# Kernel tuning notes

Measured on AMD Instinct MI355X. Metric: run time of the kernel, lower is better.

Reference implementation:

```python
import jax, jax.numpy as jnp
import numpy as np

B, BARS, BEATS, FRAC = 64, 16, 4, 8
IN_F = 10 * 47 * 2  # 940
LIN_OUT = 100
BEAT_H = 16
BAR_H = 32


def _p(key, shape, scale=0.05):
    return jax.random.normal(key, shape, dtype=jnp.float32) * scale


def setup_inputs() -> dict:
    key = jax.random.key(0)
    ks = jax.random.split(key, 16)
    return {
        "channels": jax.random.normal(ks[0], (B, BARS, BEATS, FRAC, 10, 2, 47), dtype=jnp.float32),
        "lin_w": _p(ks[1], (LIN_OUT, IN_F)),
        "lin_b": _p(ks[2], (LIN_OUT,)),
        # beats LSTM (unidirectional), PyTorch gate order i,f,g,o
        "b_wih": _p(ks[3], (4 * BEAT_H, LIN_OUT)),
        "b_whh": _p(ks[4], (4 * BEAT_H, BEAT_H)),
        "b_bih": _p(ks[5], (4 * BEAT_H,)),
        "b_bhh": _p(ks[6], (4 * BEAT_H,)),
        # bars LSTM, bidirectional: forward (f_) and reverse (r_) directions
        "f_wih": _p(ks[7], (4 * BAR_H, BEAT_H)),
        "f_whh": _p(ks[8], (4 * BAR_H, BAR_H)),
        "f_bih": _p(ks[9], (4 * BAR_H,)),
        "f_bhh": _p(ks[10], (4 * BAR_H,)),
        "r_wih": _p(ks[11], (4 * BAR_H, BEAT_H)),
        "r_whh": _p(ks[12], (4 * BAR_H, BAR_H)),
        "r_bih": _p(ks[13], (4 * BAR_H,)),
        "r_bhh": _p(ks[14], (4 * BAR_H,)),
    }


def lstm(x, wih, whh, bih, bhh):
    """PyTorch-semantics LSTM, batch_first. x: [N, T, F] -> h_seq [N, T, H]."""
    N = x.shape[0]
    H = whh.shape[1]
    # precompute input contribution for all timesteps
    xg = jnp.einsum('ntf,gf->ntg', x, wih) + (bih + bhh)  # [N, T, 4H]

    def step(carry, xt):
        h, c = carry
        gates = xt + h @ whh.T  # [N, 4H]
        i, f, g, o = jnp.split(gates, 4, axis=-1)
        c = jax.nn.sigmoid(f) * c + jax.nn.sigmoid(i) * jnp.tanh(g)
        h = jax.nn.sigmoid(o) * jnp.tanh(c)
        return (h, c), h

    h0 = jnp.zeros((N, H), x.dtype)
    _, hs = jax.lax.scan(step, (h0, h0), jnp.swapaxes(xg, 0, 1))  # [T, N, H]
    return jnp.swapaxes(hs, 0, 1)


def bilstm(x, f_wih, f_whh, f_bih, f_bhh, r_wih, r_whh, r_bih, r_bhh):
    fwd = lstm(x, f_wih, f_whh, f_bih, f_bhh)
    bwd = jnp.flip(lstm(jnp.flip(x, axis=1), r_wih, r_whh, r_bih, r_bhh), axis=1)
    return jnp.concatenate([fwd, bwd], axis=-1)


def reference(channels, lin_w, lin_b,
              b_wih, b_whh, b_bih, b_bhh,
              f_wih, f_whh, f_bih, f_bhh,
              r_wih, r_whh, r_bih, r_bhh):
    # channels: [B, bars, beats, frac, 10, 2, 47]
    x = jnp.swapaxes(channels, -1, -2)  # [..., 10, 47, 2]
    x = x.reshape(*x.shape[:4], IN_F)   # squash dims 4..6 -> 940
    x = jax.nn.relu(x @ lin_w.T + lin_b)  # [B, bars, beats, frac, 100]

    # Distributed depth=2: fold (B, bars, beats) into batch, seq over frac
    xb = x.reshape(B * BARS * BEATS, FRAC, LIN_OUT)
    beats = lstm(xb, b_wih, b_whh, b_bih, b_bhh)
    beats = beats.reshape(B, BARS, BEATS, FRAC, BEAT_H)

    # last fraction hidden state, then Distributed depth=1 over beats axis
    xl = beats[:, :, :, -1].reshape(B * BARS, BEATS, BEAT_H)
    bars = bilstm(xl, f_wih, f_whh, f_bih, f_bhh, r_wih, r_whh, r_bih, r_bhh)
    bars = bars.reshape(B, BARS, BEATS, 2 * BAR_H)
    return beats, bars
```

## Files before the change

### kernel.cpp

```cpp
#include <hip/hip_runtime.h>
#include <hip/hip_bf16.h>

typedef float f32x4 __attribute__((ext_vector_type(4)));
typedef short bf16x8 __attribute__((ext_vector_type(8)));

#define MFMA16(a, b, c) __builtin_amdgcn_mfma_f32_16x16x32_bf16(a, b, c, 0, 0, 0)

constexpr int K1      = 940;
constexpr int KP      = 960;
constexpr int NP      = 112;
constexpr int OUT1_LD = 128;

__device__ __forceinline__ float sigf(float x) { return 1.f / (1.f + __expf(-x)); }
__device__ __forceinline__ float tanhfast(float x) { return 2.f / (1.f + __expf(-2.f * x)) - 1.f; }

__device__ __forceinline__ short f2b(float x) {
  __hip_bfloat16 b = __float2bfloat16(x);
  return *reinterpret_cast<short*>(&b);
}

__global__ void prep_kernel(const float* __restrict__ lin_w,
                            const float* __restrict__ b_wih,
                            __hip_bfloat16* __restrict__ w2,
                            __hip_bfloat16* __restrict__ bw2) {
  int idx = blockIdx.x * 256 + threadIdx.x;
  if (idx < NP * KP) {
    int n = idx / KP, k = idx - n * KP;
    float v = 0.f;
    if (n < 100 && k < K1) {
      int c10 = k / 94, rem = k - c10 * 94;
      int c2 = rem / 47, c47 = rem - c2 * 47;
      int f = c10 * 94 + c47 * 2 + c2;
      v = lin_w[n * K1 + f];
    }
    w2[idx] = __float2bfloat16(v);
  } else {
    int i2 = idx - NP * KP;
    if (i2 < 64 * 128) {
      int g = i2 >> 7, k = i2 & 127;
      bw2[i2] = __float2bfloat16((k < 100) ? b_wih[g * 100 + k] : 0.f);
    }
  }
}

__global__ __launch_bounds__(256, 2)
void linear_relu_mfma(const float* __restrict__ ch,
                      const __hip_bfloat16* __restrict__ w2,
                      const float* __restrict__ lin_b,
                      __hip_bfloat16* __restrict__ out1) {
  __shared__ __align__(16) __hip_bfloat16 Bl[NP * 40];
  const int tid = threadIdx.x;
  const int wave = tid >> 6, lane = tid & 63;
  const int l16 = lane & 15, bq = lane >> 4;
  const int m0 = blockIdx.x * 64 + wave * 16;
  const long arow = (long)(m0 + l16) * K1;

  f32x4 acc[7] = {};
  for (int s = 0; s < 30; ++s) {
    const int k0 = s * 32;
    __syncthreads();
    for (int j = tid; j < 448; j += 256) {
      int n = j >> 2, q = j & 3;
      *reinterpret_cast<uint4*>(&Bl[n * 40 + q * 8]) =
          *reinterpret_cast<const uint4*>(&w2[n * KP + k0 + q * 8]);
    }
    bf16x8 a;
    if (s < 29) {
      const float4* ap = reinterpret_cast<const float4*>(&ch[arow + k0 + bq * 8]);
      float4 lo = ap[0], hi = ap[1];
      a = bf16x8{f2b(lo.x), f2b(lo.y), f2b(lo.z), f2b(lo.w),
                 f2b(hi.x), f2b(hi.y), f2b(hi.z), f2b(hi.w)};
    } else {
#pragma unroll
      for (int j = 0; j < 8; ++j) {
        int k = k0 + bq * 8 + j;
        a[j] = (k < K1) ? f2b(ch[arow + k]) : short(0);
      }
    }
    __syncthreads();
#pragma unroll
    for (int nt = 0; nt < 7; ++nt) {
      bf16x8 b = *reinterpret_cast<const bf16x8*>(&Bl[(nt * 16 + l16) * 40 + bq * 8]);
      acc[nt] = MFMA16(a, b, acc[nt]);
    }
  }
  const int mb = m0 + bq * 4;
#pragma unroll
  for (int nt = 0; nt < 7; ++nt) {
    const int n = nt * 16 + l16;
    const float bias = (n < 100) ? lin_b[n] : 0.f;
#pragma unroll
    for (int r = 0; r < 4; ++r) {
      float v = fmaxf(acc[nt][r] + bias, 0.f);
      out1[(mb + r) * OUT1_LD + n] = __float2bfloat16((n < 100) ? v : 0.f);
    }
  }
#pragma unroll
  for (int r = 0; r < 4; ++r)
    out1[(mb + r) * OUT1_LD + 112 + l16] = __float2bfloat16(0.f);
}

__global__ __launch_bounds__(256)
void xg_mfma(const __hip_bfloat16* __restrict__ out1,
             const __hip_bfloat16* __restrict__ bw2,
             const float* __restrict__ bih,
             const float* __restrict__ bhh,
             float* __restrict__ xg) {
  const int tid = threadIdx.x;
  const int wave = tid >> 6, lane = tid & 63;
  const int l16 = lane & 15, bq = lane >> 4;
  const int m0 = blockIdx.x * 64 + wave * 16;
  const int arow = (m0 + l16) * OUT1_LD;
  f32x4 acc[4] = {};
#pragma unroll
  for (int s = 0; s < 4; ++s) {
    const int k0 = s * 32;
    bf16x8 a = *reinterpret_cast<const bf16x8*>(&out1[arow + k0 + bq * 8]);
#pragma unroll
    for (int nt = 0; nt < 4; ++nt) {
      bf16x8 b = *reinterpret_cast<const bf16x8*>(&bw2[(nt * 16 + l16) * 128 + k0 + bq * 8]);
      acc[nt] = MFMA16(a, b, acc[nt]);
    }
  }
  const int mb = m0 + bq * 4;
#pragma unroll
  for (int nt = 0; nt < 4; ++nt) {
    const int g = nt * 16 + l16;
    const float bias = bih[g] + bhh[g];
#pragma unroll
    for (int r = 0; r < 4; ++r) xg[(mb + r) * 64 + g] = acc[nt][r] + bias;
  }
}

__global__ __launch_bounds__(256)
void beats_lstm(const float* __restrict__ xg,
                const float* __restrict__ whh,
                float* __restrict__ beats) {
  const int tid = threadIdx.x;
  const int sl = tid >> 6, j = tid & 63;
  const int seq = blockIdx.x * 4 + sl;
  __shared__ float hbuf[4][16];
  __shared__ float gact[4][64];
  float wr[16];
#pragma unroll
  for (int u = 0; u < 16; ++u) wr[u] = whh[j * 16 + u];
  float c = 0.f;
  if (j < 16) hbuf[sl][j] = 0.f;
  __syncthreads();
  const float* xs = xg + seq * 8 * 64;
  for (int t = 0; t < 8; ++t) {
    float pre = xs[t * 64 + j];
#pragma unroll
    for (int u = 0; u < 16; ++u) pre += wr[u] * hbuf[sl][u];
    gact[sl][j] = (j >= 32 && j < 48) ? tanhfast(pre) : sigf(pre);
    __syncthreads();
    if (j < 16) {
      c = gact[sl][16 + j] * c + gact[sl][j] * gact[sl][32 + j];
      float hn = gact[sl][48 + j] * tanhfast(c);
      hbuf[sl][j] = hn;
      beats[seq * 128 + t * 16 + j] = hn;
    }
    __syncthreads();
  }
}

__global__ __launch_bounds__(256)
void bars_bilstm(const float* __restrict__ fwih, const float* __restrict__ fwhh,
                 const float* __restrict__ fbih, const float* __restrict__ fbhh,
                 const float* __restrict__ rwih, const float* __restrict__ rwhh,
                 const float* __restrict__ rbih, const float* __restrict__ rbhh,
                 const float* __restrict__ beats,
                 float* __restrict__ bars) {
  const int tid = threadIdx.x;
  const int dir = tid >> 7, g = tid & 127;
  const int n = blockIdx.x;
  const float* wih = dir ? rwih : fwih;
  const float* whh = dir ? rwhh : fwhh;
  const float bias = dir ? (rbih[g] + rbhh[g]) : (fbih[g] + fbhh[g]);
  float wi[16], wh[32];
#pragma unroll
  for (int u = 0; u < 16; ++u) wi[u] = wih[g * 16 + u];
#pragma unroll
  for (int u = 0; u < 32; ++u) wh[u] = whh[g * 32 + u];
  __shared__ float xbuf[2][16];
  __shared__ float hbuf[2][32];
  __shared__ float gact[2][128];
  float c = 0.f;
  if (g < 32) hbuf[dir][g] = 0.f;
  __syncthreads();
  for (int t = 0; t < 4; ++t) {
    const int tt = dir ? (3 - t) : t;
    if (g < 16) xbuf[dir][g] = beats[((n * 4 + tt) * 8 + 7) * 16 + g];
    __syncthreads();
    float pre = bias;
#pragma unroll
    for (int u = 0; u < 16; ++u) pre += wi[u] * xbuf[dir][u];
#pragma unroll
    for (int u = 0; u < 32; ++u) pre += wh[u] * hbuf[dir][u];
    gact[dir][g] = (g >= 64 && g < 96) ? tanhfast(pre) : sigf(pre);
    __syncthreads();
    if (g < 32) {
      c = gact[dir][32 + g] * c + gact[dir][g] * gact[dir][64 + g];
      float hn = gact[dir][96 + g] * tanhfast(c);
      hbuf[dir][g] = hn;
      bars[(n * 4 + tt) * 64 + dir * 32 + g] = hn;
    }
    __syncthreads();
  }
}

extern "C" void kernel_launch(void* const* d_in, const int* in_sizes, int n_in,
                              void* d_out, int out_size, void* d_ws, size_t ws_size,
                              hipStream_t stream) {
  const float* ch    = (const float*)d_in[0];
  const float* lin_w = (const float*)d_in[1];
  const float* lin_b = (const float*)d_in[2];
  const float* b_wih = (const float*)d_in[3];
  const float* b_whh = (const float*)d_in[4];
  const float* b_bih = (const float*)d_in[5];
  const float* b_bhh = (const float*)d_in[6];
  const float* f_wih = (const float*)d_in[7];
  const float* f_whh = (const float*)d_in[8];
  const float* f_bih = (const float*)d_in[9];
  const float* f_bhh = (const float*)d_in[10];
  const float* r_wih = (const float*)d_in[11];
  const float* r_whh = (const float*)d_in[12];
  const float* r_bih = (const float*)d_in[13];
  const float* r_bhh = (const float*)d_in[14];

  char* ws = (char*)d_ws;
  __hip_bfloat16* w2   = (__hip_bfloat16*)ws;
  __hip_bfloat16* bw2  = (__hip_bfloat16*)(ws + 215040);
  __hip_bfloat16* out1 = (__hip_bfloat16*)(ws + 231424);
  float*          xg   = (float*)(ws + 8620032);
  float*          out  = (float*)d_out;

  prep_kernel<<<452, 256, 0, stream>>>(lin_w, b_wih, w2, bw2);
  linear_relu_mfma<<<512, 256, 0, stream>>>(ch, w2, lin_b, out1);
  xg_mfma<<<512, 256, 0, stream>>>(out1, bw2, b_bih, b_bhh, xg);
  beats_lstm<<<1024, 256, 0, stream>>>(xg, b_whh, out);
  bars_bilstm<<<1024, 256, 0, stream>>>(f_wih, f_whh, f_bih, f_bhh,
                                        r_wih, r_whh, r_bih, r_bhh,
                                        out, out + 524288);
}
```

Measured before the change: 260.7 us.

## Software-pipeline linear GEMM with direct-from-global B loads and register double buffering

The linear+ReLU MFMA kernel no longer stages the bf16 weight tile through shared memory with two barriers per K step. Each lane now loads its B fragments straight from global memory (they should hit in L2/L1), and the loop is unrolled by two with A and B prefetched one step ahead into double-buffered registers. The aim is to overlap global loads with MFMAs and remove the barrier stalls. The cost is more VGPRs under a launch bound of 2 blocks per CU, and redundant B reads across waves.

```diff
diff --git a/kernel.cpp b/kernel.cpp
--- a/kernel.cpp
+++ b/kernel.cpp
@@ -48,42 +48,64 @@
                       const __hip_bfloat16* __restrict__ w2,
                       const float* __restrict__ lin_b,
                       __hip_bfloat16* __restrict__ out1) {
-  __shared__ __align__(16) __hip_bfloat16 Bl[NP * 40];
   const int tid = threadIdx.x;
   const int wave = tid >> 6, lane = tid & 63;
   const int l16 = lane & 15, bq = lane >> 4;
   const int m0 = blockIdx.x * 64 + wave * 16;
-  const long arow = (long)(m0 + l16) * K1;
+  const float* arow = ch + (long)(m0 + l16) * K1 + bq * 8;
+  const __hip_bfloat16* brow = w2 + l16 * KP + bq * 8;
 
   f32x4 acc[7] = {};
-  for (int s = 0; s < 30; ++s) {
-    const int k0 = s * 32;
-    __syncthreads();
-    for (int j = tid; j < 448; j += 256) {
-      int n = j >> 2, q = j & 3;
-      *reinterpret_cast<uint4*>(&Bl[n * 40 + q * 8]) =
-          *reinterpret_cast<const uint4*>(&w2[n * KP + k0 + q * 8]);
-    }
+
+  auto LDA = [&](int s, float4& lo4, float4& hi4) {
+    const float* p = arow + s * 32;
+    lo4 = *reinterpret_cast<const float4*>(p);
+    hi4 = *reinterpret_cast<const float4*>(p + 4);
+  };
+  auto LDB = [&](int s, bf16x8* bb) {
+    const __hip_bfloat16* p = brow + s * 32;
+#pragma unroll
+    for (int nt = 0; nt < 7; ++nt)
+      bb[nt] = *reinterpret_cast<const bf16x8*>(p + nt * 16 * KP);
+  };
+  auto CVT = [&](float4 lo4, float4 hi4) -> bf16x8 {
+    return bf16x8{f2b(lo4.x), f2b(lo4.y), f2b(lo4.z), f2b(lo4.w),
+                  f2b(hi4.x), f2b(hi4.y), f2b(hi4.z), f2b(hi4.w)};
+  };
+  auto STEP = [&](bf16x8 a, bf16x8* bb) {
+#pragma unroll
+    for (int nt = 0; nt < 7; ++nt) acc[nt] = MFMA16(a, bb[nt], acc[nt]);
+  };
+
+  float4 l0, h0, l1, h1;
+  bf16x8 b0[7], b1[7];
+  LDA(0, l0, h0);
+  LDA(1, l1, h1);
+  LDB(0, b0);
+
+  for (int s = 0; s < 28; s += 2) {
+    bf16x8 a0 = CVT(l0, h0);
+    LDA(s + 2, l0, h0);
+    LDB(s + 1, b1);
+    STEP(a0, b0);
+    bf16x8 a1 = CVT(l1, h1);
+    if (s < 26) LDA(s + 3, l1, h1);
+    LDB(s + 2, b0);
+    STEP(a1, b1);
+  }
+  {
+    bf16x8 a = CVT(l0, h0);
+    LDB(29, b1);
+    STEP(a, b0);
+  }
+  {
     bf16x8 a;
-    if (s < 29) {
-      const float4* ap = reinterpret_cast<const float4*>(&ch[arow + k0 + bq * 8]);
-      float4 lo = ap[0], hi = ap[1];
-      a = bf16x8{f2b(lo.x), f2b(lo.y), f2b(lo.z), f2b(lo.w),
-                 f2b(hi.x), f2b(hi.y), f2b(hi.z), f2b(hi.w)};
-    } else {
-#pragma unroll
-      for (int j = 0; j < 8; ++j) {
-        int k = k0 + bq * 8 + j;
-        a[j] = (k < K1) ? f2b(ch[arow + k]) : short(0);
-      }
-    }
-    __syncthreads();
-#pragma unroll
-    for (int nt = 0; nt < 7; ++nt) {
-      bf16x8 b = *reinterpret_cast<const bf16x8*>(&Bl[(nt * 16 + l16) * 40 + bq * 8]);
-      acc[nt] = MFMA16(a, b, acc[nt]);
-    }
-  }
+#pragma unroll
+    for (int j = 0; j < 8; ++j)
+      a[j] = (928 + bq * 8 + j < K1) ? f2b(arow[928 + j]) : short(0);
+    STEP(a, b1);
+  }
+
   const int mb = m0 + bq * 4;
 #pragma unroll
   for (int nt = 0; nt < 7; ++nt) {
```

After: 269.5 us. 3.4% more time.

## Split-K linear GEMM with register-resident weights and shuffle-based beats LSTM

Applied to the files above, without the earlier changes.

The linear+ReLU GEMM becomes a split-K kernel. Each of 8 waves keeps a 128-wide K slice of the weights in registers, double-buffers A loads across four 16-row sub-tiles, and reduces the partial sums through shared memory. This removes the per-step LDS weight staging and barrier pairs of the old K-loop, but adds a 57KB shared reduction, more register pressure and extra barriers. The beats LSTM swaps its shared-memory/syncthreads recurrence for wave shuffles, with the input gates preloaded into registers.

```diff
diff --git a/kernel.cpp b/kernel.cpp
--- a/kernel.cpp
+++ b/kernel.cpp
@@ -7,7 +7,7 @@
 #define MFMA16(a, b, c) __builtin_amdgcn_mfma_f32_16x16x32_bf16(a, b, c, 0, 0, 0)
 
 constexpr int K1      = 940;
-constexpr int KP      = 960;
+constexpr int KP2     = 1024;
 constexpr int NP      = 112;
 constexpr int OUT1_LD = 128;
 
@@ -24,8 +24,8 @@
                             __hip_bfloat16* __restrict__ w2,
                             __hip_bfloat16* __restrict__ bw2) {
   int idx = blockIdx.x * 256 + threadIdx.x;
-  if (idx < NP * KP) {
-    int n = idx / KP, k = idx - n * KP;
+  if (idx < NP * KP2) {
+    int n = idx >> 10, k = idx & 1023;
     float v = 0.f;
     if (n < 100 && k < K1) {
       int c10 = k / 94, rem = k - c10 * 94;
@@ -35,7 +35,7 @@
     }
     w2[idx] = __float2bfloat16(v);
   } else {
-    int i2 = idx - NP * KP;
+    int i2 = idx - NP * KP2;
     if (i2 < 64 * 128) {
       int g = i2 >> 7, k = i2 & 127;
       bw2[i2] = __float2bfloat16((k < 100) ? b_wih[g * 100 + k] : 0.f);
@@ -43,61 +43,98 @@
   }
 }
 
-__global__ __launch_bounds__(256, 2)
-void linear_relu_mfma(const float* __restrict__ ch,
-                      const __hip_bfloat16* __restrict__ w2,
-                      const float* __restrict__ lin_b,
-                      __hip_bfloat16* __restrict__ out1) {
-  __shared__ __align__(16) __hip_bfloat16 Bl[NP * 40];
+__global__ __launch_bounds__(512, 2)
+void linear_relu_splitk(const float* __restrict__ ch,
+                        const __hip_bfloat16* __restrict__ w2,
+                        const float* __restrict__ lin_b,
+                        __hip_bfloat16* __restrict__ out1) {
+  __shared__ float red[8 * 16 * NP];
   const int tid = threadIdx.x;
-  const int wave = tid >> 6, lane = tid & 63;
+  const int w = tid >> 6, lane = tid & 63;
   const int l16 = lane & 15, bq = lane >> 4;
-  const int m0 = blockIdx.x * 64 + wave * 16;
-  const long arow = (long)(m0 + l16) * K1;
-
-  f32x4 acc[7] = {};
-  for (int s = 0; s < 30; ++s) {
-    const int k0 = s * 32;
-    __syncthreads();
-    for (int j = tid; j < 448; j += 256) {
-      int n = j >> 2, q = j & 3;
-      *reinterpret_cast<uint4*>(&Bl[n * 40 + q * 8]) =
-          *reinterpret_cast<const uint4*>(&w2[n * KP + k0 + q * 8]);
-    }
-    bf16x8 a;
-    if (s < 29) {
-      const float4* ap = reinterpret_cast<const float4*>(&ch[arow + k0 + bq * 8]);
-      float4 lo = ap[0], hi = ap[1];
-      a = bf16x8{f2b(lo.x), f2b(lo.y), f2b(lo.z), f2b(lo.w),
-                 f2b(hi.x), f2b(hi.y), f2b(hi.z), f2b(hi.w)};
+  const int kbase = w * 128;
+
+  bf16x8 breg[4][7];
+#pragma unroll
+  for (int s = 0; s < 4; ++s)
+#pragma unroll
+    for (int nt = 0; nt < 7; ++nt)
+      breg[s][nt] = *reinterpret_cast<const bf16x8*>(
+          &w2[(nt * 16 + l16) * KP2 + kbase + s * 32 + bq * 8]);
+
+  const int mbase = blockIdx.x * 64;
+
+  auto issueA = [&](int m0, float4* buf) {
+    const float* ar = ch + (long)(m0 + l16) * K1 + kbase + bq * 8;
+    if (w < 7) {
+#pragma unroll
+      for (int s = 0; s < 4; ++s) {
+        buf[2 * s]     = *reinterpret_cast<const float4*>(ar + s * 32);
+        buf[2 * s + 1] = *reinterpret_cast<const float4*>(ar + s * 32 + 4);
+      }
     } else {
+      buf[0] = *reinterpret_cast<const float4*>(ar);
+      buf[1] = *reinterpret_cast<const float4*>(ar + 4);
+      float t[8];
 #pragma unroll
       for (int j = 0; j < 8; ++j) {
-        int k = k0 + bq * 8 + j;
-        a[j] = (k < K1) ? f2b(ch[arow + k]) : short(0);
+        int k = 928 + bq * 8 + j;
+        t[j] = (k < K1) ? ar[32 + j] : 0.f;
       }
-    }
-    __syncthreads();
-#pragma unroll
-    for (int nt = 0; nt < 7; ++nt) {
-      bf16x8 b = *reinterpret_cast<const bf16x8*>(&Bl[(nt * 16 + l16) * 40 + bq * 8]);
-      acc[nt] = MFMA16(a, b, acc[nt]);
-    }
-  }
-  const int mb = m0 + bq * 4;
-#pragma unroll
-  for (int nt = 0; nt < 7; ++nt) {
-    const int n = nt * 16 + l16;
-    const float bias = (n < 100) ? lin_b[n] : 0.f;
-#pragma unroll
-    for (int r = 0; r < 4; ++r) {
-      float v = fmaxf(acc[nt][r] + bias, 0.f);
-      out1[(mb + r) * OUT1_LD + n] = __float2bfloat16((n < 100) ? v : 0.f);
-    }
-  }
-#pragma unroll
-  for (int r = 0; r < 4; ++r)
-    out1[(mb + r) * OUT1_LD + 112 + l16] = __float2bfloat16(0.f);
+      buf[2] = float4{t[0], t[1], t[2], t[3]};
+      buf[3] = float4{t[4], t[5], t[6], t[7]};
+      buf[4] = buf[5] = buf[6] = buf[7] = float4{0.f, 0.f, 0.f, 0.f};
+    }
+  };
+
+  float4 a0[8], a1[8];
+  issueA(mbase, a0);
+
+#pragma unroll
+  for (int i = 0; i < 4; ++i) {
+    float4* cur = (i & 1) ? a1 : a0;
+    float4* nxt = (i & 1) ? a0 : a1;
+    if (i < 3) issueA(mbase + (i + 1) * 16, nxt);
+
+    f32x4 acc[7] = {};
+#pragma unroll
+    for (int s = 0; s < 4; ++s) {
+      float4 lo = cur[2 * s], hi = cur[2 * s + 1];
+      bf16x8 a = bf16x8{f2b(lo.x), f2b(lo.y), f2b(lo.z), f2b(lo.w),
+                        f2b(hi.x), f2b(hi.y), f2b(hi.z), f2b(hi.w)};
+#pragma unroll
+      for (int nt = 0; nt < 7; ++nt) acc[nt] = MFMA16(a, breg[s][nt], acc[nt]);
+    }
+
+#pragma unroll
+    for (int nt = 0; nt < 7; ++nt)
+#pragma unroll
+      for (int r = 0; r < 4; ++r)
+        red[(w * 16 + bq * 4 + r) * NP + nt * 16 + l16] = acc[nt][r];
+    __syncthreads();
+
+    const int m0 = mbase + i * 16;
+    if (tid < 448) {
+      const int col = tid % NP;
+      const int rb = (tid / NP) * 4;
+      const float bias = (col < 100) ? lin_b[col] : 0.f;
+#pragma unroll
+      for (int r = 0; r < 4; ++r) {
+        float s = 0.f;
+#pragma unroll
+        for (int ww = 0; ww < 8; ++ww) s += red[(ww * 16 + rb + r) * NP + col];
+        float v = fmaxf(s + bias, 0.f);
+        out1[(m0 + rb + r) * OUT1_LD + col] = __float2bfloat16((col < 100) ? v : 0.f);
+      }
+    } else {
+      const int t2 = tid - 448;
+      const int row = t2 >> 2, c0 = 112 + (t2 & 3) * 4;
+#pragma unroll
+      for (int q = 0; q < 4; ++q)
+        out1[(m0 + row) * OUT1_LD + c0 + q] = __float2bfloat16(0.f);
+    }
+    __syncthreads();
+  }
 }
 
 __global__ __launch_bounds__(256)
@@ -136,31 +173,35 @@
 void beats_lstm(const float* __restrict__ xg,
                 const float* __restrict__ whh,
                 float* __restrict__ beats) {
-  const int tid = threadIdx.x;
-  const int sl = tid >> 6, j = tid & 63;
-  const int seq = blockIdx.x * 4 + sl;
-  __shared__ float hbuf[4][16];
-  __shared__ float gact[4][64];
+  const int lane = threadIdx.x & 63;
+  const int seq = blockIdx.x * 4 + (threadIdx.x >> 6);
+  const int cell = lane & 15;
   float wr[16];
 #pragma unroll
-  for (int u = 0; u < 16; ++u) wr[u] = whh[j * 16 + u];
+  for (int u = 0; u < 16; ++u) wr[u] = whh[lane * 16 + u];
+  const float* xs = xg + seq * 512;
+  float xv[8];
+#pragma unroll
+  for (int t = 0; t < 8; ++t) xv[t] = xs[t * 64 + lane];
+  float h[16];
+#pragma unroll
+  for (int u = 0; u < 16; ++u) h[u] = 0.f;
   float c = 0.f;
-  if (j < 16) hbuf[sl][j] = 0.f;
-  __syncthreads();
-  const float* xs = xg + seq * 8 * 64;
+#pragma unroll
   for (int t = 0; t < 8; ++t) {
-    float pre = xs[t * 64 + j];
-#pragma unroll
-    for (int u = 0; u < 16; ++u) pre += wr[u] * hbuf[sl][u];
-    gact[sl][j] = (j >= 32 && j < 48) ? tanhfast(pre) : sigf(pre);
-    __syncthreads();
-    if (j < 16) {
-      c = gact[sl][16 + j] * c + gact[sl][j] * gact[sl][32 + j];
-      float hn = gact[sl][48 + j] * tanhfast(c);
-      hbuf[sl][j] = hn;
-      beats[seq * 128 + t * 16 + j] = hn;
-    }
-    __syncthreads();
+    float pre = xv[t];
+#pragma unroll
+    for (int u = 0; u < 16; ++u) pre += wr[u] * h[u];
+    float act = (lane >= 32 && lane < 48) ? tanhfast(pre) : sigf(pre);
+    float gi = __shfl(act, cell);
+    float gf = __shfl(act, cell + 16);
+    float gg = __shfl(act, cell + 32);
+    float go = __shfl(act, cell + 48);
+    c = gf * c + gi * gg;
+    float hn = go * tanhfast(c);
+#pragma unroll
+    for (int u = 0; u < 16; ++u) h[u] = __shfl(hn, u);
+    if (lane < 16) beats[seq * 128 + t * 16 + lane] = hn;
   }
 }
 
@@ -230,13 +271,13 @@
 
   char* ws = (char*)d_ws;
   __hip_bfloat16* w2   = (__hip_bfloat16*)ws;
-  __hip_bfloat16* bw2  = (__hip_bfloat16*)(ws + 215040);
-  __hip_bfloat16* out1 = (__hip_bfloat16*)(ws + 231424);
-  float*          xg   = (float*)(ws + 8620032);
+  __hip_bfloat16* bw2  = (__hip_bfloat16*)(ws + 229376);
+  __hip_bfloat16* out1 = (__hip_bfloat16*)(ws + 245760);
+  float*          xg   = (float*)(ws + 8634368);
   float*          out  = (float*)d_out;
 
-  prep_kernel<<<452, 256, 0, stream>>>(lin_w, b_wih, w2, bw2);
-  linear_relu_mfma<<<512, 256, 0, stream>>>(ch, w2, lin_b, out1);
+  prep_kernel<<<480, 256, 0, stream>>>(lin_w, b_wih, w2, bw2);
+  linear_relu_splitk<<<512, 512, 0, stream>>>(ch, w2, lin_b, out1);
   xg_mfma<<<512, 256, 0, stream>>>(out1, bw2, b_bih, b_bhh, xg);
   beats_lstm<<<1024, 256, 0, stream>>>(xg, b_whh, out);
   bars_bilstm<<<1024, 256, 0, stream>>>(f_wih, f_whh, f_bih, f_bhh,
```

Measured after the change: 244.3 us. 1.07x faster.
